# Kernel optimization log

Measured on AMD Instinct MI355X. Metric: run time of the kernel, lower is better.

Reference implementation:

```python
import jax, jax.numpy as jnp
import numpy as np

B, C, H, W = 16, 512, 64, 64
NH = 8  # num_heads


def setup_inputs() -> dict:
    key = jax.random.key(0)
    ks = jax.random.split(key, 7)
    s = 1.0 / np.sqrt(C)
    return {
        "x": jax.random.normal(ks[0], (B, C, H, W), dtype=jnp.float32),
        "wq": jax.random.normal(ks[1], (C, C), dtype=jnp.float32) * s,
        "bq": jax.random.normal(ks[2], (C,), dtype=jnp.float32) * 0.01,
        "wk": jax.random.normal(ks[3], (C, C), dtype=jnp.float32) * s,
        "bk": jax.random.normal(ks[4], (C,), dtype=jnp.float32) * 0.01,
        "wv": jax.random.normal(ks[5], (C, C), dtype=jnp.float32) * s,
        "bv": jax.random.normal(ks[6], (C,), dtype=jnp.float32) * 0.01,
    }


def reference(x, wq, bq, wk, bk, wv, bv):
    b, c_in, h, w = x.shape
    hd = c_in // NH  # head dim

    def conv1x1(wt, bias):
        # 1x1 conv == channel GEMM: (b,c,h,w) x (o,c) -> (b,o,h,w)
        y = jnp.einsum("bchw,oc->bohw", x, wt) + bias[None, :, None, None]
        # view(b, nh, hd, h, w).permute(0,1,3,4,2) -> (b, nh, h, w, hd)
        return y.reshape(b, NH, hd, h, w).transpose(0, 1, 3, 4, 2)

    q = conv1x1(wq, bq)
    k = conv1x1(wk, bk)
    v = conv1x1(wv, bv)

    # attention along the width axis, per (batch, head, row)
    energy = jnp.einsum("bnhqc,bnhkc->bnhqk", q, k)  # (b,nh,h,w,w)
    attn = jax.nn.softmax(energy, axis=-1)
    out = jnp.einsum("bnhqk,bnhkc->bnhqc", attn, v)  # (b,nh,h,w,hd)

    # permute(0,1,4,2,3) -> (b,nh,hd,h,w) -> view(b, C, h, w)
    out = out.transpose(0, 1, 4, 2, 3).reshape(b, c_in, h, w)
    return out + x
```

## Files before the change

kernel.cpp:

```cpp
#include <hip/hip_runtime.h>
#include <stdint.h>

#define B_   16
#define C_   512
#define H_   64
#define W_   64
#define NH_  8
#define HD_  64
#define HW_  4096

typedef __attribute__((ext_vector_type(8))) _Float16 f16x8;
typedef __attribute__((ext_vector_type(8))) unsigned short u16x8;
typedef __attribute__((ext_vector_type(4))) unsigned short u16x4;
typedef __attribute__((ext_vector_type(4))) float f32x4;

static __device__ __forceinline__ unsigned short f2h(float f) {
  _Float16 h = (_Float16)f;
  unsigned short u;
  __builtin_memcpy(&u, &h, 2);
  return u;
}

static __device__ __forceinline__ void gld_lds16(const void* g, void* l) {
  __builtin_amdgcn_global_load_lds((__attribute__((address_space(1))) void*)g,
                                   (__attribute__((address_space(3))) void*)l,
                                   16, 0, 0);
}

__global__ __launch_bounds__(256) void rcca_tr(const float* __restrict__ x,
                                               unsigned short* __restrict__ xT) {
  __shared__ float lT[64 * 65];
  const int bid = blockIdx.x;
  const int st = bid & 63;
  const int ct = (bid >> 6) & 7;
  const int b  = bid >> 9;
  const int t = threadIdx.x;
  const int hwl = t & 63;
  const int cl0 = (t >> 6) * 16;
  const float* src = x + ((size_t)(b * C_ + ct * 64 + cl0)) * HW_ + st * 64 + hwl;
#pragma unroll
  for (int jj = 0; jj < 16; ++jj)
    lT[(cl0 + jj) * 65 + hwl] = src[(size_t)jj * HW_];
  __syncthreads();
  const int hw2 = t >> 2;
  const int cc0 = (t & 3) * 16;
  u16x8 o0, o1;
#pragma unroll
  for (int u = 0; u < 8; ++u) {
    o0[u] = f2h(lT[(cc0 + u) * 65 + hw2]);
    o1[u] = f2h(lT[(cc0 + 8 + u) * 65 + hw2]);
  }
  unsigned short* dst = xT + ((size_t)b * HW_ + st * 64 + hw2) * C_ + ct * 64 + cc0;
  *(u16x8*)dst = o0;
  *(u16x8*)(dst + 8) = o1;
}

__global__ __launch_bounds__(256) void rcca_cvtw(const float* __restrict__ wq,
                                                 const float* __restrict__ wk,
                                                 const float* __restrict__ wv,
                                                 unsigned short* __restrict__ Wc) {
  const int i = blockIdx.x * 256 + threadIdx.x;
  const int e = i * 4;
  const float* w = (e < 262144) ? wq : (e < 524288) ? wk : wv;
  const int off = e & 262143;
  const float4 v = *(const float4*)(w + off);
  u16x4 p;
  p[0] = f2h(v.x); p[1] = f2h(v.y); p[2] = f2h(v.z); p[3] = f2h(v.w);
  *(u16x4*)(Wc + e) = p;
}

__global__ __launch_bounds__(256) void rcca_fused(
    const unsigned short* __restrict__ xT, const unsigned short* __restrict__ Wc,
    const float* __restrict__ bq, const float* __restrict__ bk, const float* __restrict__ bv,
    const float* __restrict__ x, float* __restrict__ out) {
  __shared__ __align__(16) char smem[73728];
  const int sbid = blockIdx.x;
  const int lg = ((sbid & 7) << 9) | (sbid >> 3);
  const int head = lg & 7;
  const int bh = lg >> 3;
  const int b = bh >> 5;
  const int ht = bh & 31;
  const int t = threadIdx.x;
  const int wid = t >> 6, lane = t & 63, r = lane & 15, q = lane >> 4;
  const int wm = wid >> 1, wn = wid & 1;
  const int wbase = wid * 1024;
  const unsigned short* Abase = xT + ((size_t)b * HW_ + ht * 128) * C_;
  f32x4 acc[4][6];
#pragma unroll
  for (int i = 0; i < 4; ++i)
#pragma unroll
    for (int j = 0; j < 6; ++j) acc[i][j] = (f32x4){0.f, 0.f, 0.f, 0.f};

  auto stage = [&](char* buf, int k0) {
    char* lAb = buf;
    char* lBb = buf + 8192;
#pragma unroll
    for (int rr = 0; rr < 2; ++rr) {
      const int idx = rr * 256 + t;
      const int row = idx >> 2, ch = idx & 3;
      gld_lds16(Abase + (size_t)row * C_ + k0 + ((ch ^ (row & 3)) * 8),
                lAb + rr * 4096 + wbase);
    }
#pragma unroll
    for (int rr = 0; rr < 3; ++rr) {
      const int idx = rr * 256 + t;
      const int row = idx >> 2, ch = idx & 3;
      const int wrow = (row >> 6) * 512 + head * 64 + (row & 63);
      gld_lds16(Wc + (size_t)wrow * C_ + k0 + ((ch ^ (row & 3)) * 8),
                lBb + rr * 4096 + wbase);
    }
  };

  stage(smem, 0);
  stage(smem + 20480, 32);

#pragma unroll
  for (int tt = 0; tt < 16; ++tt) {
    if (tt < 14) stage(smem + ((tt + 2) % 3) * 20480, (tt + 2) * 32);
    if (tt < 14)      asm volatile("s_waitcnt vmcnt(10)" ::: "memory");
    else if (tt == 14) asm volatile("s_waitcnt vmcnt(5)" ::: "memory");
    else               asm volatile("s_waitcnt vmcnt(0)" ::: "memory");
    __builtin_amdgcn_s_barrier();
    const unsigned short* lA = (const unsigned short*)(smem + (tt % 3) * 20480);
    const unsigned short* lB = (const unsigned short*)(smem + (tt % 3) * 20480 + 8192);
    const int cb = q ^ (r & 3);
    f16x8 av[4], bw[6];
#pragma unroll
    for (int i = 0; i < 4; ++i)
      av[i] = *(const f16x8*)&lA[(wm * 64 + i * 16 + r) * 32 + cb * 8];
#pragma unroll
    for (int j = 0; j < 6; ++j)
      bw[j] = *(const f16x8*)&lB[(wn * 96 + j * 16 + r) * 32 + cb * 8];
    __builtin_amdgcn_s_setprio(1);
#pragma unroll
    for (int i = 0; i < 4; ++i)
#pragma unroll
      for (int j = 0; j < 6; ++j)
        acc[i][j] = __builtin_amdgcn_mfma_f32_16x16x32_f16(av[i], bw[j], acc[i][j], 0, 0, 0);
    __builtin_amdgcn_s_setprio(0);
    __builtin_amdgcn_s_barrier();
  }
  unsigned short* sQh = (unsigned short*)(smem + wm * 27648);
  unsigned short* sKh = (unsigned short*)(smem + wm * 27648 + 9216);
  unsigned short* sVh = (unsigned short*)(smem + wm * 27648 + 18432);
#pragma unroll
  for (int j = 0; j < 6; ++j) {
    const int n0 = wn * 96 + j * 16;
    const int sel = n0 >> 6;
    const int dd = (n0 & 63) + r;
    const float* bias = (sel == 0) ? bq : (sel == 1) ? bk : bv;
    const float bias_v = bias[head * 64 + dd];
    if (sel < 2) {
      unsigned short* dst = (sel == 0) ? sQh : sKh;
#pragma unroll
      for (int i = 0; i < 4; ++i)
#pragma unroll
        for (int reg = 0; reg < 4; ++reg)
          dst[(i * 16 + q * 4 + reg) * 72 + dd] = f2h(acc[i][j][reg] + bias_v);
    } else {
#pragma unroll
      for (int i = 0; i < 4; ++i) {
        u16x4 pk;
#pragma unroll
        for (int reg = 0; reg < 4; ++reg) pk[reg] = f2h(acc[i][j][reg] + bias_v);
        *(u16x4*)&sVh[dd * 72 + i * 16 + q * 4] = pk;
      }
    }
  }
  __syncthreads();
  unsigned short* sPh = (unsigned short*)(smem + 55296 + wm * 9216);
  f32x4 s2[2][4];
#pragma unroll
  for (int i2 = 0; i2 < 2; ++i2)
#pragma unroll
    for (int j = 0; j < 4; ++j) s2[i2][j] = (f32x4){0.f, 0.f, 0.f, 0.f};
#pragma unroll
  for (int kk = 0; kk < 64; kk += 32) {
    f16x8 aq0 = *(const f16x8*)&sQh[(wn * 32 + r) * 72 + kk + q * 8];
    f16x8 aq1 = *(const f16x8*)&sQh[(wn * 32 + 16 + r) * 72 + kk + q * 8];
#pragma unroll
    for (int j = 0; j < 4; ++j) {
      f16x8 bk8 = *(const f16x8*)&sKh[(j * 16 + r) * 72 + kk + q * 8];
      s2[0][j] = __builtin_amdgcn_mfma_f32_16x16x32_f16(aq0, bk8, s2[0][j], 0, 0, 0);
      s2[1][j] = __builtin_amdgcn_mfma_f32_16x16x32_f16(aq1, bk8, s2[1][j], 0, 0, 0);
    }
  }
  float inv2[2][4];
#pragma unroll
  for (int i2 = 0; i2 < 2; ++i2)
#pragma unroll
    for (int reg = 0; reg < 4; ++reg) {
      float mx = fmaxf(fmaxf(s2[i2][0][reg], s2[i2][1][reg]),
                       fmaxf(s2[i2][2][reg], s2[i2][3][reg]));
#pragma unroll
      for (int o = 1; o < 16; o <<= 1) mx = fmaxf(mx, __shfl_xor(mx, o, 64));
      float p0 = __expf(s2[i2][0][reg] - mx);
      float p1 = __expf(s2[i2][1][reg] - mx);
      float p2 = __expf(s2[i2][2][reg] - mx);
      float p3 = __expf(s2[i2][3][reg] - mx);
      float sum = p0 + p1 + p2 + p3;
#pragma unroll
      for (int o = 1; o < 16; o <<= 1) sum += __shfl_xor(sum, o, 64);
      inv2[i2][reg] = 1.0f / sum;
      const int row = wn * 32 + i2 * 16 + q * 4 + reg;
      sPh[row * 72 + r] = f2h(p0);
      sPh[row * 72 + 16 + r] = f2h(p1);
      sPh[row * 72 + 32 + r] = f2h(p2);
      sPh[row * 72 + 48 + r] = f2h(p3);
    }
  __syncthreads();
  f32x4 o4[2][4];
#pragma unroll
  for (int i2 = 0; i2 < 2; ++i2)
#pragma unroll
    for (int jd = 0; jd < 4; ++jd) o4[i2][jd] = (f32x4){0.f, 0.f, 0.f, 0.f};
#pragma unroll
  for (int kk = 0; kk < 64; kk += 32) {
    f16x8 ap0 = *(const f16x8*)&sPh[(wn * 32 + r) * 72 + kk + q * 8];
    f16x8 ap1 = *(const f16x8*)&sPh[(wn * 32 + 16 + r) * 72 + kk + q * 8];
#pragma unroll
    for (int jd = 0; jd < 4; ++jd) {
      f16x8 bv8 = *(const f16x8*)&sVh[(jd * 16 + r) * 72 + kk + q * 8];
      o4[0][jd] = __builtin_amdgcn_mfma_f32_16x16x32_f16(ap0, bv8, o4[0][jd], 0, 0, 0);
      o4[1][jd] = __builtin_amdgcn_mfma_f32_16x16x32_f16(ap1, bv8, o4[1][jd], 0, 0, 0);
    }
  }
  float* sOh = (float*)(smem + wm * 27648);
#pragma unroll
  for (int i2 = 0; i2 < 2; ++i2)
#pragma unroll
    for (int jd = 0; jd < 4; ++jd) {
      const int d = jd * 16 + r;
#pragma unroll
      for (int reg = 0; reg < 4; ++reg) {
        const int w = wn * 32 + i2 * 16 + q * 4 + reg;
        sOh[d * 66 + w] = o4[i2][jd][reg] * inv2[i2][reg];
      }
    }
  __syncthreads();
  const int d = t >> 2, w0 = (t & 3) * 16;
#pragma unroll
  for (int hs = 0; hs < 2; ++hs) {
    const float* sO2 = (const float*)(smem + hs * 27648);
    const int h = ht * 2 + hs;
    const size_t obase = (((size_t)b * C_ + head * 64 + d) * H_ + h) * (size_t)W_ + w0;
    const float4* xr = (const float4*)(x + obase);
    float4* op = (float4*)(out + obase);
#pragma unroll
    for (int u = 0; u < 4; ++u) {
      float4 xv = xr[u];
      float4 ov;
      ov.x = sO2[d * 66 + w0 + u * 4 + 0] + xv.x;
      ov.y = sO2[d * 66 + w0 + u * 4 + 1] + xv.y;
      ov.z = sO2[d * 66 + w0 + u * 4 + 2] + xv.z;
      ov.w = sO2[d * 66 + w0 + u * 4 + 3] + xv.w;
      op[u] = ov;
    }
  }
}

extern "C" void kernel_launch(void* const* d_in, const int* in_sizes, int n_in,
                              void* d_out, int out_size, void* d_ws, size_t ws_size,
                              hipStream_t stream) {
  const float* x  = (const float*)d_in[0];
  const float* wq = (const float*)d_in[1];
  const float* bq = (const float*)d_in[2];
  const float* wk = (const float*)d_in[3];
  const float* bk = (const float*)d_in[4];
  const float* wv = (const float*)d_in[5];
  const float* bv = (const float*)d_in[6];
  float* out = (float*)d_out;
  char* ws = (char*)d_ws;
  unsigned short* xT = (unsigned short*)ws;
  unsigned short* Wc = (unsigned short*)(ws + (size_t)67108864);
  hipLaunchKernelGGL(rcca_tr,    dim3(8192), dim3(256), 0, stream, x, xT);
  hipLaunchKernelGGL(rcca_cvtw,  dim3(768),  dim3(256), 0, stream, wq, wk, wv, Wc);
  hipLaunchKernelGGL(rcca_fused, dim3(4096), dim3(256), 0, stream, xT, Wc, bq, bk, bv, x, out);
}
```

Baseline: 409.2 us.

## Load weight fragments directly from global into registers, bypassing LDS staging

```diff
diff --git a/kernel.cpp b/kernel.cpp
--- a/kernel.cpp
+++ b/kernel.cpp
@@ -85,52 +85,51 @@
   const int wm = wid >> 1, wn = wid & 1;
   const int wbase = wid * 1024;
   const unsigned short* Abase = xT + ((size_t)b * HW_ + ht * 128) * C_;
+  const unsigned short* rowp[6];
+#pragma unroll
+  for (int j = 0; j < 6; ++j) {
+    const int n = wn * 96 + j * 16 + r;
+    const int wrow = (n >> 6) * 512 + head * 64 + (n & 63);
+    rowp[j] = Wc + (size_t)wrow * C_ + q * 8;
+  }
   f32x4 acc[4][6];
 #pragma unroll
   for (int i = 0; i < 4; ++i)
 #pragma unroll
     for (int j = 0; j < 6; ++j) acc[i][j] = (f32x4){0.f, 0.f, 0.f, 0.f};
 
-  auto stage = [&](char* buf, int k0) {
-    char* lAb = buf;
-    char* lBb = buf + 8192;
+  auto stageA = [&](char* buf, int k0) {
 #pragma unroll
     for (int rr = 0; rr < 2; ++rr) {
       const int idx = rr * 256 + t;
       const int row = idx >> 2, ch = idx & 3;
       gld_lds16(Abase + (size_t)row * C_ + k0 + ((ch ^ (row & 3)) * 8),
-                lAb + rr * 4096 + wbase);
-    }
-#pragma unroll
-    for (int rr = 0; rr < 3; ++rr) {
-      const int idx = rr * 256 + t;
-      const int row = idx >> 2, ch = idx & 3;
-      const int wrow = (row >> 6) * 512 + head * 64 + (row & 63);
-      gld_lds16(Wc + (size_t)wrow * C_ + k0 + ((ch ^ (row & 3)) * 8),
-                lBb + rr * 4096 + wbase);
+                buf + rr * 4096 + wbase);
     }
   };
 
-  stage(smem, 0);
-  stage(smem + 20480, 32);
+  stageA(smem, 0);
+  stageA(smem + 8192, 32);
 
 #pragma unroll
   for (int tt = 0; tt < 16; ++tt) {
-    if (tt < 14) stage(smem + ((tt + 2) % 3) * 20480, (tt + 2) * 32);
-    if (tt < 14)      asm volatile("s_waitcnt vmcnt(10)" ::: "memory");
-    else if (tt == 14) asm volatile("s_waitcnt vmcnt(5)" ::: "memory");
-    else               asm volatile("s_waitcnt vmcnt(0)" ::: "memory");
+    const int k0 = tt * 32;
+    f16x8 bw[6];
+#pragma unroll
+    for (int j = 0; j < 6; ++j)
+      bw[j] = *(const f16x8*)(rowp[j] + k0);
+    __builtin_amdgcn_sched_barrier(0);
+    if (tt < 14) stageA(smem + ((tt + 2) % 3) * 8192, (tt + 2) * 32);
+    __builtin_amdgcn_sched_barrier(0);
+    if (tt < 14) asm volatile("s_waitcnt vmcnt(2)" ::: "memory");
+    else         asm volatile("s_waitcnt vmcnt(0)" ::: "memory");
     __builtin_amdgcn_s_barrier();
-    const unsigned short* lA = (const unsigned short*)(smem + (tt % 3) * 20480);
-    const unsigned short* lB = (const unsigned short*)(smem + (tt % 3) * 20480 + 8192);
+    const unsigned short* lA = (const unsigned short*)(smem + (tt % 3) * 8192);
     const int cb = q ^ (r & 3);
-    f16x8 av[4], bw[6];
+    f16x8 av[4];
 #pragma unroll
     for (int i = 0; i < 4; ++i)
       av[i] = *(const f16x8*)&lA[(wm * 64 + i * 16 + r) * 32 + cb * 8];
-#pragma unroll
-    for (int j = 0; j < 6; ++j)
-      bw[j] = *(const f16x8*)&lB[(wn * 96 + j * 16 + r) * 32 + cb * 8];
     __builtin_amdgcn_s_setprio(1);
 #pragma unroll
     for (int i = 0; i < 4; ++i)
```

Result: slower. 506.6 us (+23.8%).
